# Kernel tuning notes

Measured on AMD Instinct MI355X. Metric: run time of the kernel, lower is better.

## Reference

```python
import jax, jax.numpy as jnp
import numpy as np

B, N, D = 2, 1024, 1024
H = 4
KD = 512          # key_dim = d_model * 0.5
VD = 1024         # value_dim = d_model
DK = KD // H      # 128 head_qk_dim
DV = VD // H      # 256 head_v_dim
LR = 16           # gate_low_rank_dim
GLN = 16.0        # gate_logit_normalizer
EPS = 1e-5


def setup_inputs() -> dict:
    key = jax.random.key(0)
    ks = jax.random.split(key, 10)
    s = 0.02
    return {
        "x": jax.random.normal(ks[0], (B, N, D), jnp.float32),
        "Wq": jax.random.normal(ks[1], (D, KD), jnp.float32) * s,
        "Wk": jax.random.normal(ks[2], (D, KD), jnp.float32) * s,
        "Wv": jax.random.normal(ks[3], (D, VD), jnp.float32) * s,
        "Wg": jax.random.normal(ks[4], (D, VD), jnp.float32) * s,
        "Wgk1": jax.random.normal(ks[5], (D, LR), jnp.float32) * s,
        "Wgk2": jax.random.normal(ks[6], (LR, KD), jnp.float32) * s,
        "bgk2": jax.random.normal(ks[7], (KD,), jnp.float32) * s,
        "Wout": jax.random.normal(ks[8], (VD, D), jnp.float32) * s,
        "rms_w": jnp.ones((DV,), jnp.float32),
    }


def _split_heads(t, h):
    b, n, hd = t.shape
    return t.reshape(b, n, h, hd // h).transpose(0, 2, 1, 3)  # b h n d


def _gla_scan(q, k, v, g):
    # q,k: [b,h,n,dk]; v: [b,h,n,dv]; g: [b,h,n,dk] (log-decay)
    b, h, n, dk = q.shape
    dv = v.shape[-1]
    qT = jnp.moveaxis(q, 2, 0)  # [n,b,h,dk]
    kT = jnp.moveaxis(k, 2, 0)
    vT = jnp.moveaxis(v, 2, 0)
    gT = jnp.moveaxis(g, 2, 0)

    def step(S, inp):
        qt, kt, vt, gt = inp
        # S_t = diag(exp(g_t)) S_{t-1} + k_t v_t^T ; o_t = q_t S_t
        S = S * jnp.exp(gt)[..., None] + kt[..., None] * vt[..., None, :]
        ot = jnp.einsum('bhk,bhkv->bhv', qt, S)
        return S, ot

    S0 = jnp.zeros((b, h, dk, dv), q.dtype)
    _, o = jax.lax.scan(step, S0, (qT, kT, vT, gT))
    return jnp.moveaxis(o, 0, 2)  # [b,h,n,dv]


def reference(x, Wq, Wk, Wv, Wg, Wgk1, Wgk2, bgk2, Wout, rms_w):
    q = _split_heads(x @ Wq, H)
    k = _split_heads(x @ Wk, H)
    v = _split_heads(x @ Wv, H)
    g = jax.nn.log_sigmoid((x @ Wgk1) @ Wgk2 + bgk2) / GLN
    g = jnp.maximum(g, -3.0)  # chunk mode clamp
    g = _split_heads(g, H)
    o = _gla_scan(q, k, v, g)               # [b,h,n,dv]
    o = o.transpose(0, 2, 1, 3)             # [b,n,h,dv]
    # RMSNorm over head_v_dim
    o = o * jax.lax.rsqrt(jnp.mean(o * o, axis=-1, keepdims=True) + EPS) * rms_w
    o = o.reshape(o.shape[0], o.shape[1], VD)
    o = o * jax.nn.silu(x @ Wg)
    return o @ Wout
```

## Files before the change

kernel.cpp:

```cpp
#include <hip/hip_runtime.h>
#include <math.h>


typedef __attribute__((ext_vector_type(4))) float vf4;
typedef __attribute__((ext_vector_type(4))) unsigned int vu4;
typedef __attribute__((ext_vector_type(8))) short short8;

#define DEVI static __device__ __forceinline__
DEVI vf4 vzero() { vf4 x = {0.f, 0.f, 0.f, 0.f}; return x; }

DEVI float bf2f(unsigned int u) {
  union { unsigned int i; float f; } c; c.i = u << 16; return c.f;
}
DEVI unsigned short f2bf(float f) {
  union { float f; unsigned int i; } c; c.f = f;
  unsigned int i = c.i;
  return (unsigned short)((i + 0x7fffu + ((i >> 16) & 1u)) >> 16);
}
DEVI void unpack8(vu4 r, float* f) {
  f[0] = bf2f(r.x & 0xffffu); f[1] = bf2f(r.x >> 16);
  f[2] = bf2f(r.y & 0xffffu); f[3] = bf2f(r.y >> 16);
  f[4] = bf2f(r.z & 0xffffu); f[5] = bf2f(r.z >> 16);
  f[6] = bf2f(r.w & 0xffffu); f[7] = bf2f(r.w >> 16);
}
DEVI vu4 pack8(const float* f) {
  vu4 o;
  o.x = (unsigned int)f2bf(f[0]) | ((unsigned int)f2bf(f[1]) << 16);
  o.y = (unsigned int)f2bf(f[2]) | ((unsigned int)f2bf(f[3]) << 16);
  o.z = (unsigned int)f2bf(f[4]) | ((unsigned int)f2bf(f[5]) << 16);
  o.w = (unsigned int)f2bf(f[6]) | ((unsigned int)f2bf(f[7]) << 16);
  return o;
}

DEVI void gld16(const unsigned short* g, unsigned short* l) {
  __builtin_amdgcn_global_load_lds(
      (const __attribute__((address_space(1))) unsigned int*)g,
      (__attribute__((address_space(3))) unsigned int*)l,
      16, 0, 0);
}

__global__ __launch_bounds__(256)
void prep_k(const float* __restrict__ Wq, const float* __restrict__ Wk,
            const float* __restrict__ Wv, const float* __restrict__ Wg,
            const float* __restrict__ Wo, const float* __restrict__ X,
            unsigned short* __restrict__ wqT, unsigned short* __restrict__ wkT,
            unsigned short* __restrict__ wvT, unsigned short* __restrict__ wgT,
            unsigned short* __restrict__ woT, unsigned short* __restrict__ xb) {
  __shared__ float T[64][65];
  const int ct = blockIdx.x, kt = blockIdx.y;
  const int t = threadIdx.x;
  const int r = t >> 2, s = t & 3;
  if (ct >= 64) {
    const int rt = ct - 64;
    const size_t base = (size_t)(rt * 64 + r) * 1024 + kt * 64 + s * 16;
    float f[16];
    *(vf4*)&f[0]  = *(const vf4*)(X + base);
    *(vf4*)&f[4]  = *(const vf4*)(X + base + 4);
    *(vf4*)&f[8]  = *(const vf4*)(X + base + 8);
    *(vf4*)&f[12] = *(const vf4*)(X + base + 12);
    *(vu4*)(xb + base) = pack8(f);
    *(vu4*)(xb + base + 8) = pack8(f + 8);
    return;
  }
  const float* W; unsigned short* O; int N; int cb;
  if (ct < 8)       { W = Wq; O = wqT; N = 512;  cb = ct; }
  else if (ct < 16) { W = Wk; O = wkT; N = 512;  cb = ct - 8; }
  else if (ct < 32) { W = Wv; O = wvT; N = 1024; cb = ct - 16; }
  else if (ct < 48) { W = Wg; O = wgT; N = 1024; cb = ct - 32; }
  else              { W = Wo; O = woT; N = 1024; cb = ct - 48; }
  const float* src = W + (size_t)(kt * 64 + r) * N + cb * 64 + s * 16;
#pragma unroll
  for (int u = 0; u < 4; ++u) {
    vf4 v4 = *(const vf4*)(src + u * 4);
    T[r][s * 16 + u * 4 + 0] = v4.x;
    T[r][s * 16 + u * 4 + 1] = v4.y;
    T[r][s * 16 + u * 4 + 2] = v4.z;
    T[r][s * 16 + u * 4 + 3] = v4.w;
  }
  __syncthreads();
  unsigned int pk[8];
#pragma unroll
  for (int u = 0; u < 8; ++u) {
    unsigned int lo = f2bf(T[s * 16 + 2 * u][r]);
    unsigned int hi = f2bf(T[s * 16 + 2 * u + 1][r]);
    pk[u] = lo | (hi << 16);
  }
  unsigned short* dst = O + (size_t)(cb * 64 + r) * 1024 + kt * 64 + s * 16;
  *(vu4*)dst = *(vu4*)&pk[0];
  *(vu4*)(dst + 8) = *(vu4*)&pk[4];
}

__global__ __launch_bounds__(256)
void proj_mfma_k(const unsigned short* __restrict__ xb,
                 const unsigned short* __restrict__ wqT, const unsigned short* __restrict__ wkT,
                 const unsigned short* __restrict__ wvT, const unsigned short* __restrict__ wgT,
                 unsigned short* __restrict__ qb, unsigned short* __restrict__ kb,
                 unsigned short* __restrict__ vb, unsigned short* __restrict__ sgb) {
  __shared__ __align__(16) unsigned short As[128 * 64];
  __shared__ __align__(16) unsigned short Bs[128 * 64];
  const int t = threadIdx.x;
  const int m0 = blockIdx.y << 7;
  const int nt = blockIdx.x;
  const unsigned short* WT; int n0; int kind;
  if (nt < 4)       { WT = wqT; n0 = nt << 7;        kind = 0; }
  else if (nt < 8)  { WT = wkT; n0 = (nt - 4) << 7;  kind = 1; }
  else if (nt < 16) { WT = wvT; n0 = (nt - 8) << 7;  kind = 2; }
  else              { WT = wgT; n0 = (nt - 16) << 7; kind = 3; }

  const int w = t >> 6, lane = t & 63;
  const int wm = (w >> 1) << 6, wn = (w & 1) << 6;
  const int qd = lane >> 4, m = lane & 15;
  const int srow = lane >> 3;
  const int scol = ((lane & 7) ^ srow) << 3;

  vf4 acc[4][4];
#pragma unroll
  for (int i = 0; i < 4; ++i)
#pragma unroll
    for (int j = 0; j < 4; ++j) acc[i][j] = vzero();

  for (int k0 = 0; k0 < 1024; k0 += 64) {
    __syncthreads();
#pragma unroll
    for (int cc = 0; cc < 4; ++cc) {
      const int c = (w << 2) + cc;
      const int row = (c << 3) + srow;
      gld16(xb + (size_t)(m0 + row) * 1024 + k0 + scol, (unsigned short*)As + (c << 9));
      gld16(WT + (size_t)(n0 + row) * 1024 + k0 + scol, (unsigned short*)Bs + (c << 9));
    }
    __syncthreads();
#pragma unroll
    for (int ks = 0; ks < 2; ++ks) {
      const int sw = (((ks << 2) + qd) ^ (m & 7)) << 3;
      short8 af[4], bf[4];
#pragma unroll
      for (int i = 0; i < 4; ++i)
        af[i] = *(const short8*)&As[(wm + i * 16 + m) * 64 + sw];
#pragma unroll
      for (int j = 0; j < 4; ++j)
        bf[j] = *(const short8*)&Bs[(wn + j * 16 + m) * 64 + sw];
#pragma unroll
      for (int i = 0; i < 4; ++i)
#pragma unroll
        for (int j = 0; j < 4; ++j)
          acc[i][j] = __builtin_amdgcn_mfma_f32_16x16x32_bf16(af[i], bf[j], acc[i][j], 0, 0, 0);
    }
  }
#pragma unroll
  for (int i = 0; i < 4; ++i) {
#pragma unroll
    for (int j = 0; j < 4; ++j) {
#pragma unroll
      for (int r = 0; r < 4; ++r) {
        const int grow = m0 + wm + i * 16 + qd * 4 + r;
        const int gcol = n0 + wn + j * 16 + m;
        float val = acc[i][j][r];
        if (kind == 0)      qb[(size_t)grow * 512 + gcol] = f2bf(val);
        else if (kind == 1) kb[(size_t)grow * 512 + gcol] = f2bf(val);
        else if (kind == 2) vb[(size_t)grow * 1024 + gcol] = f2bf(val);
        else {
          val = val / (1.f + expf(-val));
          sgb[(size_t)grow * 1024 + gcol] = f2bf(val);
        }
      }
    }
  }
}

__global__ __launch_bounds__(256)
void out_mfma_k(const unsigned short* __restrict__ Ab,
                const unsigned short* __restrict__ woT, float* __restrict__ Y) {
  __shared__ __align__(16) unsigned short As[64 * 64];
  __shared__ __align__(16) unsigned short Bs[128 * 64];
  const int t = threadIdx.x;
  const int m0 = blockIdx.y << 6;
  const int n0 = blockIdx.x << 7;
  const int w = t >> 6, lane = t & 63;
  const int wm = (w >> 1) * 32, wn = (w & 1) * 64;
  const int qd = lane >> 4, m = lane & 15;
  const int srow = lane >> 3;
  const int scol = ((lane & 7) ^ srow) << 3;

  vf4 acc[2][4];
#pragma unroll
  for (int i = 0; i < 2; ++i)
#pragma unroll
    for (int j = 0; j < 4; ++j) acc[i][j] = vzero();

  for (int k0 = 0; k0 < 1024; k0 += 64) {
    __syncthreads();
#pragma unroll
    for (int cc = 0; cc < 2; ++cc) {
      const int c = (w << 1) + cc;
      const int row = (c << 3) + srow;
      gld16(Ab + (size_t)(m0 + row) * 1024 + k0 + scol, (unsigned short*)As + (c << 9));
    }
#pragma unroll
    for (int cc = 0; cc < 4; ++cc) {
      const int c = (w << 2) + cc;
      const int row = (c << 3) + srow;
      gld16(woT + (size_t)(n0 + row) * 1024 + k0 + scol, (unsigned short*)Bs + (c << 9));
    }
    __syncthreads();
#pragma unroll
    for (int ks = 0; ks < 2; ++ks) {
      const int sw = (((ks << 2) + qd) ^ (m & 7)) << 3;
      short8 af[2], bf[4];
#pragma unroll
      for (int i = 0; i < 2; ++i)
        af[i] = *(const short8*)&As[(wm + i * 16 + m) * 64 + sw];
#pragma unroll
      for (int j = 0; j < 4; ++j)
        bf[j] = *(const short8*)&Bs[(wn + j * 16 + m) * 64 + sw];
#pragma unroll
      for (int i = 0; i < 2; ++i)
#pragma unroll
        for (int j = 0; j < 4; ++j)
          acc[i][j] = __builtin_amdgcn_mfma_f32_16x16x32_bf16(af[i], bf[j], acc[i][j], 0, 0, 0);
    }
  }
#pragma unroll
  for (int i = 0; i < 2; ++i)
#pragma unroll
    for (int j = 0; j < 4; ++j)
#pragma unroll
      for (int r = 0; r < 4; ++r) {
        const int grow = m0 + wm + i * 16 + qd * 4 + r;
        const int gcol = n0 + wn + j * 16 + m;
        Y[(size_t)grow * 1024 + gcol] = acc[i][j][r];
      }
}

__global__ __launch_bounds__(64)
void lowrank_k(const float* __restrict__ X, const float* __restrict__ W1,
               float* __restrict__ xl) {
  const int row = blockIdx.x;
  const int t = threadIdx.x;
  float acc[16];
#pragma unroll
  for (int c2 = 0; c2 < 16; ++c2) acc[c2] = 0.f;
  const float* xp = X + (size_t)row * 1024 + t * 16;
  float xv[16];
#pragma unroll
  for (int u = 0; u < 4; ++u)
    *(vf4*)&xv[u * 4] = *(const vf4*)(xp + u * 4);
#pragma unroll
  for (int j = 0; j < 16; ++j) {
    const float* wp = W1 + (size_t)(t * 16 + j) * 16;
    float wv[16];
#pragma unroll
    for (int u = 0; u < 4; ++u)
      *(vf4*)&wv[u * 4] = *(const vf4*)(wp + u * 4);
#pragma unroll
    for (int c2 = 0; c2 < 16; ++c2) acc[c2] = fmaf(xv[j], wv[c2], acc[c2]);
  }
#pragma unroll
  for (int mm = 1; mm < 64; mm <<= 1) {
#pragma unroll
    for (int c2 = 0; c2 < 16; ++c2) acc[c2] += __shfl_xor(acc[c2], mm, 64);
  }
  if (t == 0) {
#pragma unroll
    for (int c2 = 0; c2 < 16; ++c2) xl[(size_t)row * 16 + c2] = acc[c2];
  }
}

__global__ __launch_bounds__(256)
void gate_scan_k(const float* __restrict__ xl, const float* __restrict__ W2,
                 const float* __restrict__ bias,
                 unsigned short* __restrict__ q, unsigned short* __restrict__ k,
                 float* __restrict__ ebtot) {
  const int t = threadIdx.x;
  const int w = t >> 6, lane = t & 63;
  const int wid = blockIdx.x * 4 + w;
  const int kt = wid & 31;
  const int c = (wid >> 5) & 15;
  const int b = wid >> 9;
  const int kbase = kt * 16;
  const size_t rowbase = (size_t)b * 1024 + c * 64;

  const float* xp = xl + (rowbase + lane) * 16;
  float xv[16];
#pragma unroll
  for (int u = 0; u < 4; ++u)
    *(vf4*)&xv[u * 4] = *(const vf4*)(xp + u * 4);

  const size_t a = (rowbase + lane) * 512 + kbase;
  vu4 qr0 = *(const vu4*)(q + a), qr1 = *(const vu4*)(q + a + 8);
  vu4 kr0 = *(const vu4*)(k + a), kr1 = *(const vu4*)(k + a + 8);
  float qf[16], kf[16];
  unpack8(qr0, qf); unpack8(qr1, qf + 8);
  unpack8(kr0, kf); unpack8(kr1, kf + 8);

  float gf[16];
#pragma unroll
  for (int cc = 0; cc < 16; ++cc) {
    const int col = kbase + cc;
    float z = bias[col];
#pragma unroll
    for (int j = 0; j < 16; ++j) z = fmaf(xv[j], W2[j * 512 + col], z);
    float ls = fminf(z, 0.f) - log1pf(expf(-fabsf(z)));
    float g = fmaxf(ls * (1.f / 16.f), -3.f);
#pragma unroll
    for (int d = 1; d < 64; d <<= 1) {
      float up = __shfl_up(g, d, 64);
      if (lane >= d) g += up;
    }
    qf[cc] *= expf(g);
    kf[cc] *= expf(fminf(-g, 80.f));
    gf[cc] = g;
  }
  *(vu4*)(q + a) = pack8(qf);
  *(vu4*)(q + a + 8) = pack8(qf + 8);
  *(vu4*)(k + a) = pack8(kf);
  *(vu4*)(k + a + 8) = pack8(kf + 8);
  if (lane == 63) {
    float* ep = ebtot + ((size_t)b * 16 + c) * 512 + kbase;
#pragma unroll
    for (int cc = 0; cc < 16; ++cc) ep[cc] = expf(gf[cc]);
  }
}

__global__ __launch_bounds__(256)
void intra_kv_k(const unsigned short* __restrict__ q16, const unsigned short* __restrict__ k16,
                const unsigned short* __restrict__ v, float* __restrict__ o,
                unsigned short* __restrict__ ST) {
  __shared__ __align__(16) unsigned short Qs[64 * 136];
  __shared__ __align__(16) unsigned short Ks[64 * 136];
  __shared__ __align__(16) unsigned short Kt[128 * 68];
  __shared__ __align__(16) unsigned short Vt[128 * 68];
  __shared__ __align__(16) unsigned short Asb[64 * 68];
  const int t = threadIdx.x;
  const int vh = blockIdx.x, c = blockIdx.y, bh = blockIdx.z;
  const int b = bh >> 2, h = bh & 3;
  const size_t rowbase = (size_t)b * 1024 + c * 64;

#pragma unroll
  for (int u2 = 0; u2 < 4; ++u2) {
    const int id = t + (u2 << 8);
    const int row = id >> 4, kg = id & 15;
    vu4 rq = *(const vu4*)(q16 + (rowbase + row) * 512 + h * 128 + kg * 8);
    *(vu4*)&Qs[row * 136 + kg * 8] = rq;
    vu4 rk = *(const vu4*)(k16 + (rowbase + row) * 512 + h * 128 + kg * 8);
    *(vu4*)&Ks[row * 136 + kg * 8] = rk;
    const unsigned short* kp = (const unsigned short*)&rk;
#pragma unroll
    for (int u = 0; u < 8; ++u)
      Kt[(kg * 8 + u) * 68 + row] = kp[u];
    vu4 rv = *(const vu4*)(v + (rowbase + row) * 1024 + h * 256 + vh * 128 + kg * 8);
    const unsigned short* vp = (const unsigned short*)&rv;
#pragma unroll
    for (int u = 0; u < 8; ++u)
      Vt[(kg * 8 + u) * 68 + row] = vp[u];
  }
  __syncthreads();

  const int w = t >> 6, lane = t & 63;
  const int qd = lane >> 4, m = lane & 15;

  {
    short8 af[4];
#pragma unroll
    for (int kf = 0; kf < 4; ++kf)
      af[kf] = *(const short8*)&Qs[(w * 16 + m) * 136 + kf * 32 + qd * 8];
    vf4 acc[4];
#pragma unroll
    for (int jt = 0; jt < 4; ++jt) acc[jt] = vzero();
#pragma unroll
    for (int jt = 0; jt < 4; ++jt)
#pragma unroll
      for (int kf = 0; kf < 4; ++kf) {
        short8 bfr = *(const short8*)&Ks[(jt * 16 + m) * 136 + kf * 32 + qd * 8];
        acc[jt] = __builtin_amdgcn_mfma_f32_16x16x32_bf16(af[kf], bfr, acc[jt], 0, 0, 0);
      }
#pragma unroll
    for (int jt = 0; jt < 4; ++jt)
#pragma unroll
      for (int r = 0; r < 4; ++r) {
        const int i = w * 16 + qd * 4 + r;
        const int j = jt * 16 + m;
        Asb[i * 68 + j] = f2bf((j <= i) ? acc[jt][r] : 0.f);
      }
  }
  __syncthreads();

  {
    vf4 acc2[4][2];
#pragma unroll
    for (int mt = 0; mt < 4; ++mt) { acc2[mt][0] = vzero(); acc2[mt][1] = vzero(); }
#pragma unroll
    for (int kf = 0; kf < 2; ++kf) {
      short8 bf0 = *(const short8*)&Vt[(w * 32 + m) * 68 + kf * 32 + qd * 8];
      short8 bf1 = *(const short8*)&Vt[(w * 32 + 16 + m) * 68 + kf * 32 + qd * 8];
#pragma unroll
      for (int mt = 0; mt < 4; ++mt) {
        short8 af = *(const short8*)&Asb[(mt * 16 + m) * 68 + kf * 32 + qd * 8];
        acc2[mt][0] = __builtin_amdgcn_mfma_f32_16x16x32_bf16(af, bf0, acc2[mt][0], 0, 0, 0);
        acc2[mt][1] = __builtin_amdgcn_mfma_f32_16x16x32_bf16(af, bf1, acc2[mt][1], 0, 0, 0);
      }
    }
#pragma unroll
    for (int mt = 0; mt < 4; ++mt)
#pragma unroll
      for (int nt = 0; nt < 2; ++nt)
#pragma unroll
        for (int r = 0; r < 4; ++r) {
          const int i = mt * 16 + qd * 4 + r;
          const int vc = h * 256 + vh * 128 + w * 32 + nt * 16 + m;
          o[(rowbase + i) * 1024 + vc] = acc2[mt][nt][r];
        }
  }

  {
    short8 af3[2][2];
#pragma unroll
    for (int mt = 0; mt < 2; ++mt)
#pragma unroll
      for (int kf = 0; kf < 2; ++kf)
        af3[mt][kf] = *(const short8*)&Vt[(w * 32 + mt * 16 + m) * 68 + kf * 32 + qd * 8];
#pragma unroll
    for (int nt = 0; nt < 8; ++nt) {
      vf4 a0 = vzero(), a1 = vzero();
#pragma unroll
      for (int kf = 0; kf < 2; ++kf) {
        short8 bfr = *(const short8*)&Kt[(nt * 16 + m) * 68 + kf * 32 + qd * 8];
        a0 = __builtin_amdgcn_mfma_f32_16x16x32_bf16(af3[0][kf], bfr, a0, 0, 0, 0);
        a1 = __builtin_amdgcn_mfma_f32_16x16x32_bf16(af3[1][kf], bfr, a1, 0, 0, 0);
      }
      const size_t sbase = (size_t)(bh * 16 + c) * 256 + vh * 128 + w * 32;
#pragma unroll
      for (int r = 0; r < 4; ++r) {
        ST[(sbase + qd * 4 + r) * 128 + nt * 16 + m] = f2bf(a0[r]);
        ST[(sbase + 16 + qd * 4 + r) * 128 + nt * 16 + m] = f2bf(a1[r]);
      }
    }
  }
}

__global__ __launch_bounds__(256)
void state_scan_k(unsigned short* __restrict__ ST, const float* __restrict__ ebtot) {
  const int idx = blockIdx.x * 256 + threadIdx.x;
  const int kg = idx & 15;
  const int vv = (idx >> 4) & 255;
  const int bh = idx >> 12;
  const int b = bh >> 2, h = bh & 3;
  float s[8];
#pragma unroll
  for (int u = 0; u < 8; ++u) s[u] = 0.f;
  for (int c = 0; c < 16; ++c) {
    unsigned short* p = ST + ((size_t)(bh * 16 + c) * 256 + vv) * 128 + kg * 8;
    const float* ep = ebtot + ((size_t)b * 16 + c) * 512 + h * 128 + kg * 8;
    float e[8];
    *(vf4*)&e[0] = *(const vf4*)ep;
    *(vf4*)&e[4] = *(const vf4*)(ep + 4);
    float kv[8];
    unpack8(*(const vu4*)p, kv);
    *(vu4*)p = pack8(s);
#pragma unroll
    for (int u = 0; u < 8; ++u) s[u] = (s[u] + kv[u]) * e[u];
  }
}

__global__ __launch_bounds__(256)
void o_inter_k(const unsigned short* __restrict__ q16, const unsigned short* __restrict__ ST,
               float* __restrict__ o) {
  __shared__ __align__(16) unsigned short Qs[64 * 136];
  __shared__ __align__(16) unsigned short Ss[128 * 136];
  const int t = threadIdx.x;
  const int vt = blockIdx.x, c = blockIdx.y, bh = blockIdx.z;
  const int b = bh >> 2, h = bh & 3;
  const size_t rowbase = (size_t)b * 1024 + c * 64;

#pragma unroll
  for (int u2 = 0; u2 < 4; ++u2) {
    const int id = t + (u2 << 8);
    const int row = id >> 4, kg = id & 15;
    *(vu4*)&Qs[row * 136 + kg * 8] =
        *(const vu4*)(q16 + (rowbase + row) * 512 + h * 128 + kg * 8);
  }
#pragma unroll
  for (int u2 = 0; u2 < 8; ++u2) {
    const int id = t + (u2 << 8);
    const int vrow = id >> 4, kg = id & 15;
    *(vu4*)&Ss[vrow * 136 + kg * 8] =
        *(const vu4*)(ST + ((size_t)(bh * 16 + c) * 256 + vt * 128 + vrow) * 128 + kg * 8);
  }
  __syncthreads();

  const int w = t >> 6, lane = t & 63;
  const int qd = lane >> 4, m = lane & 15;
  short8 af[4];
#pragma unroll
  for (int kf = 0; kf < 4; ++kf)
    af[kf] = *(const short8*)&Qs[(w * 16 + m) * 136 + kf * 32 + qd * 8];
#pragma unroll
  for (int nt = 0; nt < 8; ++nt) {
    vf4 acc = vzero();
#pragma unroll
    for (int kf = 0; kf < 4; ++kf) {
      short8 bfr = *(const short8*)&Ss[(nt * 16 + m) * 136 + kf * 32 + qd * 8];
      acc = __builtin_amdgcn_mfma_f32_16x16x32_bf16(af[kf], bfr, acc, 0, 0, 0);
    }
    float* base = o + (rowbase + w * 16 + qd * 4) * 1024 + h * 256 + vt * 128 + nt * 16 + m;
#pragma unroll
    for (int r = 0; r < 4; ++r)
      base[(size_t)r * 1024] += acc[r];
  }
}

__global__ __launch_bounds__(256)
void norm_gate_k(const float* __restrict__ o, const float* __restrict__ rmsw,
                 const unsigned short* __restrict__ sg,
                 unsigned short* __restrict__ ob) {
  __shared__ float red[4];
  const int grp = blockIdx.x;
  const int row = grp >> 2, h = grp & 3;
  const int t = threadIdx.x;
  const size_t idx = (size_t)row * 1024 + h * 256 + t;
  const float val = o[idx];
  float ss = val * val;
#pragma unroll
  for (int mm = 1; mm < 64; mm <<= 1) ss += __shfl_xor(ss, mm, 64);
  if ((t & 63) == 0) red[t >> 6] = ss;
  __syncthreads();
  const float tot = red[0] + red[1] + red[2] + red[3];
  const float scale = rsqrtf(tot * (1.f / 256.f) + 1e-5f);
  ob[idx] = f2bf(val * scale * rmsw[t] * bf2f((unsigned int)sg[idx]));
}

extern "C" void kernel_launch(void* const* d_in, const int* in_sizes, int n_in,
                              void* d_out, int out_size, void* d_ws, size_t ws_size,
                              hipStream_t stream) {
  const float* x    = (const float*)d_in[0];
  const float* Wq   = (const float*)d_in[1];
  const float* Wk   = (const float*)d_in[2];
  const float* Wv   = (const float*)d_in[3];
  const float* Wg   = (const float*)d_in[4];
  const float* Wgk1 = (const float*)d_in[5];
  const float* Wgk2 = (const float*)d_in[6];
  const float* bgk2 = (const float*)d_in[7];
  const float* Wout = (const float*)d_in[8];
  const float* rmsw = (const float*)d_in[9];

  const size_t MB = 1u << 20;
  char* w = (char*)d_ws;
  unsigned short* qb16   = (unsigned short*)(w);
  unsigned short* kb16   = (unsigned short*)(w + 2 * MB);
  unsigned short* vbuf   = (unsigned short*)(w + 4 * MB);
  unsigned short* sgbuf  = (unsigned short*)(w + 8 * MB);
  float*          obuf   = (float*)(w + 12 * MB);
  char*           sreg   = w + 20 * MB;
  unsigned short* xb     = (unsigned short*)sreg;
  unsigned short* STbuf  = (unsigned short*)sreg;
  unsigned short* obuf_b = (unsigned short*)sreg;
  float*          xlbuf  = (float*)(w + 28 * MB);
  float*          ebbuf  = (float*)(w + 28 * MB + 131072);
  unsigned short* wqT    = (unsigned short*)(w + 29 * MB);
  unsigned short* wkT    = (unsigned short*)(w + 30 * MB);
  unsigned short* wvT    = (unsigned short*)(w + 31 * MB);
  unsigned short* wgT    = (unsigned short*)(w + 33 * MB);
  unsigned short* woT    = (unsigned short*)(w + 35 * MB);

  prep_k<<<dim3(96, 16), 256, 0, stream>>>(Wq, Wk, Wv, Wg, Wout, x,
                                           wqT, wkT, wvT, wgT, woT, xb);
  lowrank_k<<<2048, 64, 0, stream>>>(x, Wgk1, xlbuf);
  proj_mfma_k<<<dim3(24, 16), 256, 0, stream>>>(xb, wqT, wkT, wvT, wgT, qb16, kb16, vbuf, sgbuf);
  gate_scan_k<<<256, 256, 0, stream>>>(xlbuf, Wgk2, bgk2, qb16, kb16, ebbuf);
  intra_kv_k<<<dim3(2, 16, 8), 256, 0, stream>>>(qb16, kb16, vbuf, obuf, STbuf);
  state_scan_k<<<128, 256, 0, stream>>>(STbuf, ebbuf);
  o_inter_k<<<dim3(2, 16, 8), 256, 0, stream>>>(qb16, STbuf, obuf);
  norm_gate_k<<<8192, 256, 0, stream>>>(obuf, rmsw, sgbuf, obuf_b);
  out_mfma_k<<<dim3(8, 32), 256, 0, stream>>>(obuf_b, woT, (float*)d_out);
}
```

Before: 194.2 us.

## Regroup prep kernels and vectorize norm-gate to cut small-kernel overhead

Splits the combined prep kernel into a weight-transpose kernel that handles two 64x64 tiles per block, and a kernel that fuses the x-to-bf16 conversion with the low-rank gate projection, which packs four rows per 256-thread block instead of one row per 64-thread block. The RMSNorm/gate kernel now gives each wave one head-row and loads four elements per lane, removing the shared-memory reduction and the barrier. The aim is fewer, fuller blocks and wider memory accesses in the memory-bound prologue and epilogue kernels. The out_mfma kernel is only moved in the file.

```diff
diff --git a/kernel.cpp b/kernel.cpp
--- a/kernel.cpp
+++ b/kernel.cpp
@@ -5,6 +5,7 @@
 typedef __attribute__((ext_vector_type(4))) float vf4;
 typedef __attribute__((ext_vector_type(4))) unsigned int vu4;
 typedef __attribute__((ext_vector_type(8))) short short8;
+typedef __attribute__((ext_vector_type(4))) unsigned short us4;
 
 #define DEVI static __device__ __forceinline__
 DEVI vf4 vzero() { vf4 x = {0.f, 0.f, 0.f, 0.f}; return x; }
@@ -40,19 +41,61 @@
 }
 
 __global__ __launch_bounds__(256)
-void prep_k(const float* __restrict__ Wq, const float* __restrict__ Wk,
-            const float* __restrict__ Wv, const float* __restrict__ Wg,
-            const float* __restrict__ Wo, const float* __restrict__ X,
-            unsigned short* __restrict__ wqT, unsigned short* __restrict__ wkT,
-            unsigned short* __restrict__ wvT, unsigned short* __restrict__ wgT,
-            unsigned short* __restrict__ woT, unsigned short* __restrict__ xb) {
-  __shared__ float T[64][65];
-  const int ct = blockIdx.x, kt = blockIdx.y;
+void wtrans_k(const float* __restrict__ Wq, const float* __restrict__ Wk,
+              const float* __restrict__ Wv, const float* __restrict__ Wg,
+              const float* __restrict__ Wo,
+              unsigned short* __restrict__ wqT, unsigned short* __restrict__ wkT,
+              unsigned short* __restrict__ wvT, unsigned short* __restrict__ wgT,
+              unsigned short* __restrict__ woT) {
+  __shared__ float T[2][64][65];
   const int t = threadIdx.x;
   const int r = t >> 2, s = t & 3;
-  if (ct >= 64) {
-    const int rt = ct - 64;
-    const size_t base = (size_t)(rt * 64 + r) * 1024 + kt * 64 + s * 16;
+  float f[2][16];
+  const float* srcs[2];
+  unsigned short* dsts[2];
+#pragma unroll
+  for (int i = 0; i < 2; ++i) {
+    const int tid = blockIdx.x * 2 + i;
+    const float* W; unsigned short* O; int kt, cb, N;
+    if (tid < 128)       { W = Wq; O = wqT; N = 512;  kt = tid >> 3;          cb = tid & 7;  }
+    else if (tid < 256)  { W = Wk; O = wkT; N = 512;  kt = (tid - 128) >> 3;  cb = tid & 7;  }
+    else if (tid < 512)  { W = Wv; O = wvT; N = 1024; kt = (tid - 256) >> 4;  cb = tid & 15; }
+    else if (tid < 768)  { W = Wg; O = wgT; N = 1024; kt = (tid - 512) >> 4;  cb = tid & 15; }
+    else                 { W = Wo; O = woT; N = 1024; kt = (tid - 768) >> 4;  cb = tid & 15; }
+    srcs[i] = W + (size_t)(kt * 64 + r) * N + cb * 64 + s * 16;
+    dsts[i] = O + (size_t)(cb * 64 + r) * 1024 + kt * 64 + s * 16;
+  }
+#pragma unroll
+  for (int i = 0; i < 2; ++i)
+#pragma unroll
+    for (int u = 0; u < 4; ++u)
+      *(vf4*)&f[i][u * 4] = *(const vf4*)(srcs[i] + u * 4);
+#pragma unroll
+  for (int i = 0; i < 2; ++i)
+#pragma unroll
+    for (int u = 0; u < 16; ++u)
+      T[i][r][s * 16 + u] = f[i][u];
+  __syncthreads();
+#pragma unroll
+  for (int i = 0; i < 2; ++i) {
+    unsigned int pk[8];
+#pragma unroll
+    for (int u = 0; u < 8; ++u) {
+      unsigned int lo = f2bf(T[i][s * 16 + 2 * u][r]);
+      unsigned int hi = f2bf(T[i][s * 16 + 2 * u + 1][r]);
+      pk[u] = lo | (hi << 16);
+    }
+    *(vu4*)dsts[i] = *(vu4*)&pk[0];
+    *(vu4*)(dsts[i] + 8) = *(vu4*)&pk[4];
+  }
+}
+
+__global__ __launch_bounds__(256)
+void xcvt_lr_k(const float* __restrict__ X, const float* __restrict__ Wgk1,
+               unsigned short* __restrict__ xb, float* __restrict__ xl) {
+  const int bid = blockIdx.x, t = threadIdx.x;
+  if (bid < 512) {
+    const size_t base = (size_t)bid * 4096 + t * 16;
     float f[16];
     *(vf4*)&f[0]  = *(const vf4*)(X + base);
     *(vf4*)&f[4]  = *(const vf4*)(X + base + 4);
@@ -62,32 +105,35 @@
     *(vu4*)(xb + base + 8) = pack8(f + 8);
     return;
   }
-  const float* W; unsigned short* O; int N; int cb;
-  if (ct < 8)       { W = Wq; O = wqT; N = 512;  cb = ct; }
-  else if (ct < 16) { W = Wk; O = wkT; N = 512;  cb = ct - 8; }
-  else if (ct < 32) { W = Wv; O = wvT; N = 1024; cb = ct - 16; }
-  else if (ct < 48) { W = Wg; O = wgT; N = 1024; cb = ct - 32; }
-  else              { W = Wo; O = woT; N = 1024; cb = ct - 48; }
-  const float* src = W + (size_t)(kt * 64 + r) * N + cb * 64 + s * 16;
-#pragma unroll
-  for (int u = 0; u < 4; ++u) {
-    vf4 v4 = *(const vf4*)(src + u * 4);
-    T[r][s * 16 + u * 4 + 0] = v4.x;
-    T[r][s * 16 + u * 4 + 1] = v4.y;
-    T[r][s * 16 + u * 4 + 2] = v4.z;
-    T[r][s * 16 + u * 4 + 3] = v4.w;
-  }
-  __syncthreads();
-  unsigned int pk[8];
-#pragma unroll
-  for (int u = 0; u < 8; ++u) {
-    unsigned int lo = f2bf(T[s * 16 + 2 * u][r]);
-    unsigned int hi = f2bf(T[s * 16 + 2 * u + 1][r]);
-    pk[u] = lo | (hi << 16);
-  }
-  unsigned short* dst = O + (size_t)(cb * 64 + r) * 1024 + kt * 64 + s * 16;
-  *(vu4*)dst = *(vu4*)&pk[0];
-  *(vu4*)(dst + 8) = *(vu4*)&pk[4];
+  const int w = t >> 6, lane = t & 63;
+  const int row = (bid - 512) * 4 + w;
+  float acc[16];
+#pragma unroll
+  for (int c2 = 0; c2 < 16; ++c2) acc[c2] = 0.f;
+  const float* xp = X + (size_t)row * 1024 + lane * 16;
+  float xv[16];
+#pragma unroll
+  for (int u = 0; u < 4; ++u)
+    *(vf4*)&xv[u * 4] = *(const vf4*)(xp + u * 4);
+#pragma unroll
+  for (int j = 0; j < 16; ++j) {
+    const float* wp = Wgk1 + (size_t)(lane * 16 + j) * 16;
+    float wv[16];
+#pragma unroll
+    for (int u = 0; u < 4; ++u)
+      *(vf4*)&wv[u * 4] = *(const vf4*)(wp + u * 4);
+#pragma unroll
+    for (int c2 = 0; c2 < 16; ++c2) acc[c2] = fmaf(xv[j], wv[c2], acc[c2]);
+  }
+#pragma unroll
+  for (int mm = 1; mm < 64; mm <<= 1) {
+#pragma unroll
+    for (int c2 = 0; c2 < 16; ++c2) acc[c2] += __shfl_xor(acc[c2], mm, 64);
+  }
+  if (lane == 0) {
+#pragma unroll
+    for (int c2 = 0; c2 < 16; ++c2) xl[(size_t)row * 16 + c2] = acc[c2];
+  }
 }
 
 __global__ __launch_bounds__(256)
@@ -168,104 +214,6 @@
 }
 
 __global__ __launch_bounds__(256)
-void out_mfma_k(const unsigned short* __restrict__ Ab,
-                const unsigned short* __restrict__ woT, float* __restrict__ Y) {
-  __shared__ __align__(16) unsigned short As[64 * 64];
-  __shared__ __align__(16) unsigned short Bs[128 * 64];
-  const int t = threadIdx.x;
-  const int m0 = blockIdx.y << 6;
-  const int n0 = blockIdx.x << 7;
-  const int w = t >> 6, lane = t & 63;
-  const int wm = (w >> 1) * 32, wn = (w & 1) * 64;
-  const int qd = lane >> 4, m = lane & 15;
-  const int srow = lane >> 3;
-  const int scol = ((lane & 7) ^ srow) << 3;
-
-  vf4 acc[2][4];
-#pragma unroll
-  for (int i = 0; i < 2; ++i)
-#pragma unroll
-    for (int j = 0; j < 4; ++j) acc[i][j] = vzero();
-
-  for (int k0 = 0; k0 < 1024; k0 += 64) {
-    __syncthreads();
-#pragma unroll
-    for (int cc = 0; cc < 2; ++cc) {
-      const int c = (w << 1) + cc;
-      const int row = (c << 3) + srow;
-      gld16(Ab + (size_t)(m0 + row) * 1024 + k0 + scol, (unsigned short*)As + (c << 9));
-    }
-#pragma unroll
-    for (int cc = 0; cc < 4; ++cc) {
-      const int c = (w << 2) + cc;
-      const int row = (c << 3) + srow;
-      gld16(woT + (size_t)(n0 + row) * 1024 + k0 + scol, (unsigned short*)Bs + (c << 9));
-    }
-    __syncthreads();
-#pragma unroll
-    for (int ks = 0; ks < 2; ++ks) {
-      const int sw = (((ks << 2) + qd) ^ (m & 7)) << 3;
-      short8 af[2], bf[4];
-#pragma unroll
-      for (int i = 0; i < 2; ++i)
-        af[i] = *(const short8*)&As[(wm + i * 16 + m) * 64 + sw];
-#pragma unroll
-      for (int j = 0; j < 4; ++j)
-        bf[j] = *(const short8*)&Bs[(wn + j * 16 + m) * 64 + sw];
-#pragma unroll
-      for (int i = 0; i < 2; ++i)
-#pragma unroll
-        for (int j = 0; j < 4; ++j)
-          acc[i][j] = __builtin_amdgcn_mfma_f32_16x16x32_bf16(af[i], bf[j], acc[i][j], 0, 0, 0);
-    }
-  }
-#pragma unroll
-  for (int i = 0; i < 2; ++i)
-#pragma unroll
-    for (int j = 0; j < 4; ++j)
-#pragma unroll
-      for (int r = 0; r < 4; ++r) {
-        const int grow = m0 + wm + i * 16 + qd * 4 + r;
-        const int gcol = n0 + wn + j * 16 + m;
-        Y[(size_t)grow * 1024 + gcol] = acc[i][j][r];
-      }
-}
-
-__global__ __launch_bounds__(64)
-void lowrank_k(const float* __restrict__ X, const float* __restrict__ W1,
-               float* __restrict__ xl) {
-  const int row = blockIdx.x;
-  const int t = threadIdx.x;
-  float acc[16];
-#pragma unroll
-  for (int c2 = 0; c2 < 16; ++c2) acc[c2] = 0.f;
-  const float* xp = X + (size_t)row * 1024 + t * 16;
-  float xv[16];
-#pragma unroll
-  for (int u = 0; u < 4; ++u)
-    *(vf4*)&xv[u * 4] = *(const vf4*)(xp + u * 4);
-#pragma unroll
-  for (int j = 0; j < 16; ++j) {
-    const float* wp = W1 + (size_t)(t * 16 + j) * 16;
-    float wv[16];
-#pragma unroll
-    for (int u = 0; u < 4; ++u)
-      *(vf4*)&wv[u * 4] = *(const vf4*)(wp + u * 4);
-#pragma unroll
-    for (int c2 = 0; c2 < 16; ++c2) acc[c2] = fmaf(xv[j], wv[c2], acc[c2]);
-  }
-#pragma unroll
-  for (int mm = 1; mm < 64; mm <<= 1) {
-#pragma unroll
-    for (int c2 = 0; c2 < 16; ++c2) acc[c2] += __shfl_xor(acc[c2], mm, 64);
-  }
-  if (t == 0) {
-#pragma unroll
-    for (int c2 = 0; c2 < 16; ++c2) xl[(size_t)row * 16 + c2] = acc[c2];
-  }
-}
-
-__global__ __launch_bounds__(256)
 void gate_scan_k(const float* __restrict__ xl, const float* __restrict__ W2,
                  const float* __restrict__ bias,
                  unsigned short* __restrict__ q, unsigned short* __restrict__ k,
@@ -512,20 +460,88 @@
 void norm_gate_k(const float* __restrict__ o, const float* __restrict__ rmsw,
                  const unsigned short* __restrict__ sg,
                  unsigned short* __restrict__ ob) {
-  __shared__ float red[4];
-  const int grp = blockIdx.x;
+  const int t = threadIdx.x;
+  const int w = t >> 6, lane = t & 63;
+  const int grp = blockIdx.x * 4 + w;
   const int row = grp >> 2, h = grp & 3;
-  const int t = threadIdx.x;
-  const size_t idx = (size_t)row * 1024 + h * 256 + t;
-  const float val = o[idx];
-  float ss = val * val;
+  const size_t base = (size_t)row * 1024 + h * 256 + lane * 4;
+  vf4 val = *(const vf4*)(o + base);
+  float ss = val.x * val.x + val.y * val.y + val.z * val.z + val.w * val.w;
 #pragma unroll
   for (int mm = 1; mm < 64; mm <<= 1) ss += __shfl_xor(ss, mm, 64);
-  if ((t & 63) == 0) red[t >> 6] = ss;
-  __syncthreads();
-  const float tot = red[0] + red[1] + red[2] + red[3];
-  const float scale = rsqrtf(tot * (1.f / 256.f) + 1e-5f);
-  ob[idx] = f2bf(val * scale * rmsw[t] * bf2f((unsigned int)sg[idx]));
+  const float scale = rsqrtf(ss * (1.f / 256.f) + 1e-5f);
+  us4 sgv = *(const us4*)(sg + base);
+  vf4 rw = *(const vf4*)(rmsw + lane * 4);
+  us4 outv;
+  outv.x = f2bf(val.x * scale * rw.x * bf2f((unsigned int)sgv.x));
+  outv.y = f2bf(val.y * scale * rw.y * bf2f((unsigned int)sgv.y));
+  outv.z = f2bf(val.z * scale * rw.z * bf2f((unsigned int)sgv.z));
+  outv.w = f2bf(val.w * scale * rw.w * bf2f((unsigned int)sgv.w));
+  *(us4*)(ob + base) = outv;
+}
+
+__global__ __launch_bounds__(256)
+void out_mfma_k(const unsigned short* __restrict__ Ab,
+                const unsigned short* __restrict__ woT, float* __restrict__ Y) {
+  __shared__ __align__(16) unsigned short As[64 * 64];
+  __shared__ __align__(16) unsigned short Bs[128 * 64];
+  const int t = threadIdx.x;
+  const int m0 = blockIdx.y << 6;
+  const int n0 = blockIdx.x << 7;
+  const int w = t >> 6, lane = t & 63;
+  const int wm = (w >> 1) * 32, wn = (w & 1) * 64;
+  const int qd = lane >> 4, m = lane & 15;
+  const int srow = lane >> 3;
+  const int scol = ((lane & 7) ^ srow) << 3;
+
+  vf4 acc[2][4];
+#pragma unroll
+  for (int i = 0; i < 2; ++i)
+#pragma unroll
+    for (int j = 0; j < 4; ++j) acc[i][j] = vzero();
+
+  for (int k0 = 0; k0 < 1024; k0 += 64) {
+    __syncthreads();
+#pragma unroll
+    for (int cc = 0; cc < 2; ++cc) {
+      const int c = (w << 1) + cc;
+      const int row = (c << 3) + srow;
+      gld16(Ab + (size_t)(m0 + row) * 1024 + k0 + scol, (unsigned short*)As + (c << 9));
+    }
+#pragma unroll
+    for (int cc = 0; cc < 4; ++cc) {
+      const int c = (w << 2) + cc;
+      const int row = (c << 3) + srow;
+      gld16(woT + (size_t)(n0 + row) * 1024 + k0 + scol, (unsigned short*)Bs + (c << 9));
+    }
+    __syncthreads();
+#pragma unroll
+    for (int ks = 0; ks < 2; ++ks) {
+      const int sw = (((ks << 2) + qd) ^ (m & 7)) << 3;
+      short8 af[2], bf[4];
+#pragma unroll
+      for (int i = 0; i < 2; ++i)
+        af[i] = *(const short8*)&As[(wm + i * 16 + m) * 64 + sw];
+#pragma unroll
+      for (int j = 0; j < 4; ++j)
+        bf[j] = *(const short8*)&Bs[(wn + j * 16 + m) * 64 + sw];
+#pragma unroll
+      for (int i = 0; i < 2; ++i)
+#pragma unroll
+        for (int j = 0; j < 4; ++j)
+          acc[i][j] = __builtin_amdgcn_mfma_f32_16x16x32_bf16(af[i], bf[j], acc[i][j], 0, 0, 0);
+    }
+  }
+#pragma unroll
+  for (int i = 0; i < 2; ++i)
+#pragma unroll
+    for (int j = 0; j < 4; ++j)
+#pragma unroll
+      for (int r = 0; r < 4; ++r) {
+        const int grow = m0 + wm + i * 16 + qd * 4 + r;
+        const int gcol = n0 + wn + j * 16 + m;
+        Y[(size_t)grow * 1024 + gcol] = acc[i][j][r];
+      }
 }
 
 extern "C" void kernel_launch(void* const* d_in, const int* in_sizes, int n_in,
@@ -561,14 +577,13 @@
   unsigned short* wgT    = (unsigned short*)(w + 33 * MB);
   unsigned short* woT    = (unsigned short*)(w + 35 * MB);
 
-  prep_k<<<dim3(96, 16), 256, 0, stream>>>(Wq, Wk, Wv, Wg, Wout, x,
-                                           wqT, wkT, wvT, wgT, woT, xb);
-  lowrank_k<<<2048, 64, 0, stream>>>(x, Wgk1, xlbuf);
+  wtrans_k<<<512, 256, 0, stream>>>(Wq, Wk, Wv, Wg, Wout, wqT, wkT, wvT, wgT, woT);
+  xcvt_lr_k<<<1024, 256, 0, stream>>>(x, Wgk1, xb, xlbuf);
   proj_mfma_k<<<dim3(24, 16), 256, 0, stream>>>(xb, wqT, wkT, wvT, wgT, qb16, kb16, vbuf, sgbuf);
   gate_scan_k<<<256, 256, 0, stream>>>(xlbuf, Wgk2, bgk2, qb16, kb16, ebbuf);
   intra_kv_k<<<dim3(2, 16, 8), 256, 0, stream>>>(qb16, kb16, vbuf, obuf, STbuf);
   state_scan_k<<<128, 256, 0, stream>>>(STbuf, ebbuf);
   o_inter_k<<<dim3(2, 16, 8), 256, 0, stream>>>(qb16, STbuf, obuf);
-  norm_gate_k<<<8192, 256, 0, stream>>>(obuf, rmsw, sgbuf, obuf_b);
+  norm_gate_k<<<2048, 256, 0, stream>>>(obuf, rmsw, sgbuf, obuf_b);
   out_mfma_k<<<dim3(8, 32), 256, 0, stream>>>(obuf_b, woT, (float*)d_out);
 }
```

Result: no change. 194.4 us (+0.1%).
